# Optimization experiments

Hardware: AMD Instinct MI355X
Metric: run time of the kernel (lower is better)

Reference implementation:

```python
import jax, jax.numpy as jnp
import numpy as np

NUM_EXPERTS = 8
TOP_K = 2


def setup_inputs() -> dict:
    key = jax.random.key(0)
    k1, k2, k3, k4, k5 = jax.random.split(key, 5)
    B, S, H, F, E = 4, 2048, 1024, 4096, NUM_EXPERTS
    return {
        "hidden_states": jax.random.normal(k1, (B, S, H), dtype=jnp.float32),
        "gate_w": jax.random.normal(k2, (E, H), dtype=jnp.float32) * 0.02,
        "w1": jax.random.normal(k3, (E, F, H), dtype=jnp.float32) * 0.02,
        "w3": jax.random.normal(k4, (E, F, H), dtype=jnp.float32) * 0.02,
        "w2": jax.random.normal(k5, (E, H, F), dtype=jnp.float32) * 0.02,
    }


def reference(hidden_states, gate_w, w1, w3, w2):
    B, S, H = hidden_states.shape
    E = gate_w.shape[0]
    x = hidden_states.reshape(-1, H)  # [T, H]
    T = x.shape[0]

    # Router: logits -> fp32 softmax -> top-k -> renormalize (Mixtral)
    router_logits = x @ gate_w.T  # [T, E]
    probs = jax.nn.softmax(router_logits.astype(jnp.float32), axis=-1)
    top_w, top_idx = jax.lax.top_k(probs, TOP_K)  # [T, K]
    top_w = top_w / jnp.sum(top_w, axis=-1, keepdims=True)
    top_w = top_w.astype(x.dtype)

    # Combine weights per (token, expert); zero for unselected experts.
    comb = jnp.zeros((T, E), dtype=x.dtype).at[
        jnp.arange(T)[:, None], top_idx
    ].add(top_w)  # [T, E]

    out = jnp.zeros((T, H), dtype=x.dtype)
    for e in range(E):  # structural loop over distinct expert weights
        h = jax.nn.silu(x @ w1[e].T) * (x @ w3[e].T)  # [T, F]
        out = out + comb[:, e:e + 1] * (h @ w2[e].T)  # [T, H]

    return out.reshape(B, S, H), router_logits
```

## Files before the change

### kernel.cpp

```cpp
#include <hip/hip_runtime.h>
#include <hip/hip_bf16.h>
#include <stdint.h>

#define T_TOK 8192
#define H_DIM 1024
#define F_DIM 4096
#define NEXP  8
#define CAP        17408
#define CT128      136

typedef __attribute__((ext_vector_type(8))) short bf16x8;
typedef __attribute__((ext_vector_type(4))) float f32x4;

#define AS1 __attribute__((address_space(1)))
#define AS3 __attribute__((address_space(3)))

__device__ __forceinline__ void gload_lds16(const void* g, void* l) {
  __builtin_amdgcn_global_load_lds((const AS1 void*)g, (AS3 void*)l, 16, 0, 0);
}

struct TK { int i0, i1; float w0, w1; };

__global__ __launch_bounds__(256) void router_kernel(
    const float* __restrict__ x, const float* __restrict__ gw,
    float* __restrict__ logits, int* __restrict__ counts, TK* __restrict__ tk)
{
  const int lane = threadIdx.x & 63;
  const int t = blockIdx.x * 4 + (threadIdx.x >> 6);
  const float* xp = x + (size_t)t * H_DIM;
  float xr[16];
#pragma unroll
  for (int i = 0; i < 16; ++i) xr[i] = xp[lane + i * 64];
  float lg[NEXP];
#pragma unroll
  for (int e = 0; e < NEXP; ++e) {
    const float* gp = gw + e * H_DIM;
    float acc = 0.f;
#pragma unroll
    for (int i = 0; i < 16; ++i) acc += xr[i] * gp[lane + i * 64];
#pragma unroll
    for (int s = 32; s > 0; s >>= 1) acc += __shfl_xor(acc, s, 64);
    lg[e] = acc;
  }
  if (lane < NEXP) logits[(size_t)t * NEXP + lane] = lg[lane];
  if (lane == 0) {
    int i0 = 0; float m0 = lg[0];
#pragma unroll
    for (int e = 1; e < NEXP; ++e) if (lg[e] > m0) { m0 = lg[e]; i0 = e; }
    int i1 = -1; float m1 = -1e30f;
#pragma unroll
    for (int e = 0; e < NEXP; ++e) if (e != i0 && lg[e] > m1) { m1 = lg[e]; i1 = e; }
    float r = expf(m1 - m0);
    float w0 = 1.f / (1.f + r);
    float w1 = r / (1.f + r);
    TK v; v.i0 = i0; v.i1 = i1; v.w0 = w0; v.w1 = w1;
    tk[t] = v;
    atomicAdd(&counts[i0], 1);
    atomicAdd(&counts[i1], 1);
  }
}

__global__ __launch_bounds__(256) void scan_kernel(
    const int* __restrict__ counts, int* __restrict__ offs,
    int* __restrict__ cursor, int* __restrict__ tile_expert)
{
  __shared__ int so[NEXP + 1];
  const int tid = threadIdx.x;
  if (tid == 0) {
    int o = 0;
    for (int e = 0; e < NEXP; ++e) {
      so[e] = o; offs[e] = o; cursor[e] = o;
      o += (counts[e] + 127) & ~127;
    }
    so[NEXP] = o; offs[NEXP] = o;
  }
  __syncthreads();
  for (int ti = tid; ti < CT128; ti += 256) {
    int row = ti * 128;
    int e = NEXP - 1;
#pragma unroll
    for (int k = 0; k < NEXP; ++k)
      if (row >= so[k] && row < so[k + 1]) { e = k; break; }
    tile_expert[ti] = e;
  }
}

__global__ __launch_bounds__(256) void scatter_kernel(
    const TK* __restrict__ tk, int* __restrict__ cursor,
    int* __restrict__ pair_tok, float* __restrict__ pair_w,
    int2* __restrict__ inv)
{
  int t = blockIdx.x * 256 + threadIdx.x;
  if (t >= T_TOK) return;
  TK v = tk[t];
  int p0 = atomicAdd(&cursor[v.i0], 1);
  pair_tok[p0] = t; pair_w[p0] = v.w0;
  int p1 = atomicAdd(&cursor[v.i1], 1);
  pair_tok[p1] = t; pair_w[p1] = v.w1;
  inv[t] = make_int2(p0, p1);
}

union Pack8 { __hip_bfloat16 o[8]; uint4 u; };

__global__ __launch_bounds__(256) void gather_kernel(
    const float* __restrict__ x, const int* __restrict__ pair_tok,
    __hip_bfloat16* __restrict__ xg)
{
  int idx = blockIdx.x * 256 + threadIdx.x;
  int row = idx >> 7;
  int c8  = (idx & 127) << 3;
  int tok = pair_tok[row];
  const float4* src = reinterpret_cast<const float4*>(x + (size_t)tok * H_DIM + c8);
  float4 a = src[0], b = src[1];
  Pack8 pk;
  pk.o[0] = __float2bfloat16(a.x); pk.o[1] = __float2bfloat16(a.y);
  pk.o[2] = __float2bfloat16(a.z); pk.o[3] = __float2bfloat16(a.w);
  pk.o[4] = __float2bfloat16(b.x); pk.o[5] = __float2bfloat16(b.y);
  pk.o[6] = __float2bfloat16(b.z); pk.o[7] = __float2bfloat16(b.w);
  *reinterpret_cast<uint4*>(xg + (size_t)row * H_DIM + c8) = pk.u;
}

__global__ __launch_bounds__(256) void convert3_kernel(
    const float* __restrict__ w1, const float* __restrict__ w3,
    const float* __restrict__ w2, __hip_bfloat16* __restrict__ w1b,
    __hip_bfloat16* __restrict__ w3b, __hip_bfloat16* __restrict__ w2b)
{
  const long long nthr = 3ll * (1 << 22);
  for (long long idx = (long long)blockIdx.x * 256 + threadIdx.x; idx < nthr;
       idx += (long long)gridDim.x * 256) {
    int seg = (int)(idx >> 22);
    long long off = (idx & ((1 << 22) - 1)) * 8;
    const float* src = (seg == 0) ? w1 : (seg == 1) ? w3 : w2;
    __hip_bfloat16* dst = (seg == 0) ? w1b : (seg == 1) ? w3b : w2b;
    float4 a = *reinterpret_cast<const float4*>(src + off);
    float4 b = *reinterpret_cast<const float4*>(src + off + 4);
    Pack8 pk;
    pk.o[0] = __float2bfloat16(a.x); pk.o[1] = __float2bfloat16(a.y);
    pk.o[2] = __float2bfloat16(a.z); pk.o[3] = __float2bfloat16(a.w);
    pk.o[4] = __float2bfloat16(b.x); pk.o[5] = __float2bfloat16(b.y);
    pk.o[6] = __float2bfloat16(b.z); pk.o[7] = __float2bfloat16(b.w);
    *reinterpret_cast<uint4*>(dst + off) = pk.u;
  }
}


__global__ __launch_bounds__(256, 4) void gemm1_kernel(
    const __hip_bfloat16* __restrict__ xg,
    const __hip_bfloat16* __restrict__ w1b,
    const __hip_bfloat16* __restrict__ w3b,
    const int* __restrict__ tile_expert,
    __hip_bfloat16* __restrict__ h)
{
  __shared__ __hip_bfloat16 smem[16384];
  __hip_bfloat16* sA  = smem;
  __hip_bfloat16* sB1 = smem + 8192;
  __hip_bfloat16* sB3 = smem + 12288;

  const int n_  = blockIdx.x;
  const int tm  = n_ >> 6;
  const int tf  = n_ & 63;
  const int e   = tile_expert[tm];
  const int tid = threadIdx.x;

  const __hip_bfloat16* A  = xg  + (size_t)tm * 128 * H_DIM;
  const __hip_bfloat16* B1 = w1b + (size_t)e * F_DIM * H_DIM + (size_t)tf * 64 * H_DIM;
  const __hip_bfloat16* B3 = w3b + (size_t)e * F_DIM * H_DIM + (size_t)tf * 64 * H_DIM;

  const int rs  = tid >> 3;
  const int sl  = tid & 7;
  const int xsl = (sl ^ (rs & 7)) * 8;
  const int dst = rs * 64 + sl * 8;

  const int wv = tid >> 6, lane = tid & 63;
  const int wm = wv >> 1, wn = wv & 1;
  const int l16 = lane & 15, lk = lane >> 4;
  const int ps0 = ((0 + lk) ^ (l16 & 7)) * 8;
  const int ps1 = ((4 + lk) ^ (l16 & 7)) * 8;

  f32x4 acc1[4][2] = {};
  f32x4 acc3[4][2] = {};

  for (int kt = 0; kt < H_DIM / 64; ++kt) {
    __syncthreads();
    const int gk = kt * 64 + xsl;
#pragma unroll
    for (int c = 0; c < 4; ++c)
      gload_lds16(A + (size_t)(rs + 32 * c) * H_DIM + gk, &sA[c * 2048 + dst]);
#pragma unroll
    for (int c = 0; c < 2; ++c) {
      gload_lds16(B1 + (size_t)(rs + 32 * c) * H_DIM + gk, &sB1[c * 2048 + dst]);
      gload_lds16(B3 + (size_t)(rs + 32 * c) * H_DIM + gk, &sB3[c * 2048 + dst]);
    }
    __syncthreads();
#pragma unroll
    for (int ks = 0; ks < 2; ++ks) {
      const int ps = ks ? ps1 : ps0;
      bf16x8 a[4], b1[2], b3[2];
#pragma unroll
      for (int m = 0; m < 4; ++m)
        a[m] = *reinterpret_cast<const bf16x8*>(&sA[(wm * 64 + m * 16 + l16) * 64 + ps]);
#pragma unroll
      for (int nf = 0; nf < 2; ++nf) {
        b1[nf] = *reinterpret_cast<const bf16x8*>(&sB1[(wn * 32 + nf * 16 + l16) * 64 + ps]);
        b3[nf] = *reinterpret_cast<const bf16x8*>(&sB3[(wn * 32 + nf * 16 + l16) * 64 + ps]);
      }
#pragma unroll
      for (int m = 0; m < 4; ++m)
#pragma unroll
        for (int nf = 0; nf < 2; ++nf) {
          acc1[m][nf] = __builtin_amdgcn_mfma_f32_16x16x32_bf16(a[m], b1[nf], acc1[m][nf], 0, 0, 0);
          acc3[m][nf] = __builtin_amdgcn_mfma_f32_16x16x32_bf16(a[m], b3[nf], acc3[m][nf], 0, 0, 0);
        }
    }
  }

  __syncthreads();
#pragma unroll
  for (int m = 0; m < 4; ++m)
#pragma unroll
    for (int nf = 0; nf < 2; ++nf)
#pragma unroll
      for (int j = 0; j < 4; ++j) {
        int row = wm * 64 + m * 16 + lk * 4 + j;
        int col = wn * 32 + nf * 16 + l16;
        int phys = row * 64 + (((col >> 3) ^ (row & 7)) << 3) + (col & 7);
        float c1 = acc1[m][nf][j];
        float c3 = acc3[m][nf][j];
        float s  = c1 / (1.f + expf(-c1));
        smem[phys] = __float2bfloat16(s * c3);
      }
  __syncthreads();
  const uint4* s4 = reinterpret_cast<const uint4*>(smem);
  __hip_bfloat16* hp = h + (size_t)tm * 128 * F_DIM + (size_t)tf * 64;
#pragma unroll
  for (int i = 0; i < 4; ++i) {
    int c = i * 256 + tid;
    int row = c >> 3, sg = c & 7;
    *reinterpret_cast<uint4*>(hp + (size_t)row * F_DIM + sg * 8) =
        s4[row * 8 + (sg ^ (row & 7))];
  }
}

__global__ __launch_bounds__(256, 4) void gemm2_kernel(
    const __hip_bfloat16* __restrict__ h,
    const __hip_bfloat16* __restrict__ w2b,
    const int* __restrict__ tile_expert,
    const float* __restrict__ pair_w,
    __hip_bfloat16* __restrict__ y)
{
  __shared__ __hip_bfloat16 smem[16384];
  __hip_bfloat16* sA = smem;
  __hip_bfloat16* sB = smem + 8192;

  const int n_  = blockIdx.x;
  const int tn  = n_ & 7;
  const int tm  = n_ >> 3;
  const int e   = tile_expert[tm];
  const int tid = threadIdx.x;

  const __hip_bfloat16* A = h   + (size_t)tm * 128 * F_DIM;
  const __hip_bfloat16* B = w2b + (size_t)e * H_DIM * F_DIM + (size_t)tn * 128 * F_DIM;

  const int rs  = tid >> 3;
  const int sl  = tid & 7;
  const int xsl = (sl ^ (rs & 7)) * 8;
  const int dst = rs * 64 + sl * 8;

  const int wv = tid >> 6, lane = tid & 63;
  const int wm = wv >> 1, wn = wv & 1;
  const int l16 = lane & 15, lk = lane >> 4;
  const int ps0 = ((0 + lk) ^ (l16 & 7)) * 8;
  const int ps1 = ((4 + lk) ^ (l16 & 7)) * 8;

  f32x4 acc[4][4] = {};

  for (int kt = 0; kt < F_DIM / 64; ++kt) {
    __syncthreads();
    const int gk = kt * 64 + xsl;
#pragma unroll
    for (int c = 0; c < 4; ++c) {
      gload_lds16(A + (size_t)(rs + 32 * c) * F_DIM + gk, &sA[c * 2048 + dst]);
      gload_lds16(B + (size_t)(rs + 32 * c) * F_DIM + gk, &sB[c * 2048 + dst]);
    }
    __syncthreads();
#pragma unroll
    for (int ks = 0; ks < 2; ++ks) {
      const int ps = ks ? ps1 : ps0;
      bf16x8 a[4], b[4];
#pragma unroll
      for (int m = 0; m < 4; ++m)
        a[m] = *reinterpret_cast<const bf16x8*>(&sA[(wm * 64 + m * 16 + l16) * 64 + ps]);
#pragma unroll
      for (int nf = 0; nf < 4; ++nf)
        b[nf] = *reinterpret_cast<const bf16x8*>(&sB[(wn * 64 + nf * 16 + l16) * 64 + ps]);
#pragma unroll
      for (int m = 0; m < 4; ++m)
#pragma unroll
        for (int nf = 0; nf < 4; ++nf)
          acc[m][nf] = __builtin_amdgcn_mfma_f32_16x16x32_bf16(a[m], b[nf], acc[m][nf], 0, 0, 0);
    }
  }

  __syncthreads();
#pragma unroll
  for (int m = 0; m < 4; ++m)
#pragma unroll
    for (int j = 0; j < 4; ++j) {
      int row  = wm * 64 + m * 16 + lk * 4 + j;
      float w  = pair_w[tm * 128 + row];
#pragma unroll
      for (int nf = 0; nf < 4; ++nf) {
        int col  = wn * 64 + nf * 16 + l16;
        int phys = row * 128 + (((col >> 3) ^ (row & 7)) << 3) + (col & 7);
        smem[phys] = __float2bfloat16(w * acc[m][nf][j]);
      }
    }
  __syncthreads();
  const uint4* s4 = reinterpret_cast<const uint4*>(smem);
  __hip_bfloat16* yp = y + (size_t)tm * 128 * H_DIM + (size_t)tn * 128;
#pragma unroll
  for (int i = 0; i < 8; ++i) {
    int c = i * 256 + tid;
    int row = c >> 4, sg = c & 15;
    *reinterpret_cast<uint4*>(yp + (size_t)row * H_DIM + sg * 8) =
        s4[row * 16 + ((sg & 8) | ((sg ^ row) & 7))];
  }
}

__global__ __launch_bounds__(256) void combine_kernel(
    const __hip_bfloat16* __restrict__ y, const int2* __restrict__ inv,
    float* __restrict__ out)
{
  int idx = blockIdx.x * 256 + threadIdx.x;
  int t  = idx >> 7;
  int c8 = (idx & 127) << 3;
  int2 p = inv[t];
  union { uint4 u; __hip_bfloat16 o[8]; } a, b;
  a.u = *reinterpret_cast<const uint4*>(y + (size_t)p.x * H_DIM + c8);
  b.u = *reinterpret_cast<const uint4*>(y + (size_t)p.y * H_DIM + c8);
  float4 o0, o1;
  o0.x = __bfloat162float(a.o[0]) + __bfloat162float(b.o[0]);
  o0.y = __bfloat162float(a.o[1]) + __bfloat162float(b.o[1]);
  o0.z = __bfloat162float(a.o[2]) + __bfloat162float(b.o[2]);
  o0.w = __bfloat162float(a.o[3]) + __bfloat162float(b.o[3]);
  o1.x = __bfloat162float(a.o[4]) + __bfloat162float(b.o[4]);
  o1.y = __bfloat162float(a.o[5]) + __bfloat162float(b.o[5]);
  o1.z = __bfloat162float(a.o[6]) + __bfloat162float(b.o[6]);
  o1.w = __bfloat162float(a.o[7]) + __bfloat162float(b.o[7]);
  float* op = out + (size_t)t * H_DIM + c8;
  *reinterpret_cast<float4*>(op)     = o0;
  *reinterpret_cast<float4*>(op + 4) = o1;
}

#define WS_COUNTS   0
#define WS_CURSOR   32
#define WS_OFFS     64
#define WS_TILEEXP  128
#define WS_TK       1024
#define WS_PAIRTOK  132096
#define WS_PAIRW    201728
#define WS_ZERO_BYTES 271360
#define WS_INV      271360
#define WS_XG       336896ll
#define WS_W1       (WS_XG + 35651584ll)
#define WS_W3       (WS_W1 + 67108864ll)
#define WS_W2       (WS_W3 + 67108864ll)
#define WS_H        (WS_W2 + 67108864ll)
#define WS_Y        WS_XG

extern "C" void kernel_launch(void* const* d_in, const int* in_sizes, int n_in,
                              void* d_out, int out_size, void* d_ws, size_t ws_size,
                              hipStream_t stream) {
  const float* x  = (const float*)d_in[0];
  const float* gw = (const float*)d_in[1];
  const float* w1 = (const float*)d_in[2];
  const float* w3 = (const float*)d_in[3];
  const float* w2 = (const float*)d_in[4];
  float* out    = (float*)d_out;
  float* logits = out + (size_t)T_TOK * H_DIM;

  char* ws = (char*)d_ws;
  int*   counts   = (int*)(ws + WS_COUNTS);
  int*   cursor   = (int*)(ws + WS_CURSOR);
  int*   offs     = (int*)(ws + WS_OFFS);
  int*   tile_exp = (int*)(ws + WS_TILEEXP);
  TK*    tk       = (TK*)(ws + WS_TK);
  int*   pair_tok = (int*)(ws + WS_PAIRTOK);
  float* pair_w   = (float*)(ws + WS_PAIRW);
  int2*  inv      = (int2*)(ws + WS_INV);
  __hip_bfloat16* xg  = (__hip_bfloat16*)(ws + WS_XG);
  __hip_bfloat16* w1b = (__hip_bfloat16*)(ws + WS_W1);
  __hip_bfloat16* w3b = (__hip_bfloat16*)(ws + WS_W3);
  __hip_bfloat16* w2b = (__hip_bfloat16*)(ws + WS_W2);
  __hip_bfloat16* hbuf = (__hip_bfloat16*)(ws + WS_H);
  __hip_bfloat16* ybuf = (__hip_bfloat16*)(ws + WS_Y);

  hipMemsetAsync(d_ws, 0, WS_ZERO_BYTES, stream);

  convert3_kernel<<<8192, 256, 0, stream>>>(w1, w3, w2, w1b, w3b, w2b);

  router_kernel<<<T_TOK / 4, 256, 0, stream>>>(x, gw, logits, counts, tk);
  scan_kernel<<<1, 256, 0, stream>>>(counts, offs, cursor, tile_exp);
  scatter_kernel<<<T_TOK / 256, 256, 0, stream>>>(tk, cursor, pair_tok, pair_w, inv);
  gather_kernel<<<(CAP * 128) / 256, 256, 0, stream>>>(x, pair_tok, xg);

  gemm1_kernel<<<CT128 * (F_DIM / 64), 256, 0, stream>>>(
      xg, w1b, w3b, tile_exp, hbuf);
  gemm2_kernel<<<CT128 * (H_DIM / 128), 256, 0, stream>>>(
      hbuf, w2b, tile_exp, pair_w, ybuf);
  combine_kernel<<<(T_TOK * H_DIM / 8) / 256, 256, 0, stream>>>(ybuf, inv, out);
}
```

Before: 899.4 us.

## Split-K gemm2 into two halves and sum partials in combine kernel

Splits the second expert GEMM's K dimension (F=4096) into two halves, doubling the grid from 1088 to 2176 blocks. Each half writes its own bf16 partial output buffer, and the combine kernel now reads four partials per token instead of two. Block indices are also remapped so that consecutive blocks share groups of 8 M-tiles, which is meant to improve L2 reuse. The cost is double the y traffic, an extra bf16 rounding of each partial, and a second y buffer placed in the workspace after the first, which must fit in the existing allocation.

```diff
diff --git a/kernel.cpp b/kernel.cpp
--- a/kernel.cpp
+++ b/kernel.cpp
@@ -253,13 +253,18 @@
   __hip_bfloat16* sB = smem + 8192;
 
   const int n_  = blockIdx.x;
-  const int tn  = n_ & 7;
-  const int tm  = n_ >> 3;
+  const int r   = n_ & 7;
+  const int q   = n_ >> 3;
+  const int tm  = (q >> 4) * 8 + r;
+  const int s_  = q & 15;
+  const int tn  = s_ >> 1;
+  const int kh  = s_ & 1;
   const int e   = tile_expert[tm];
   const int tid = threadIdx.x;
 
-  const __hip_bfloat16* A = h   + (size_t)tm * 128 * F_DIM;
-  const __hip_bfloat16* B = w2b + (size_t)e * H_DIM * F_DIM + (size_t)tn * 128 * F_DIM;
+  const __hip_bfloat16* A = h   + (size_t)tm * 128 * F_DIM + (size_t)kh * 2048;
+  const __hip_bfloat16* B = w2b + (size_t)e * H_DIM * F_DIM + (size_t)tn * 128 * F_DIM
+                                + (size_t)kh * 2048;
 
   const int rs  = tid >> 3;
   const int sl  = tid & 7;
@@ -274,7 +279,7 @@
 
   f32x4 acc[4][4] = {};
 
-  for (int kt = 0; kt < F_DIM / 64; ++kt) {
+  for (int kt = 0; kt < 2048 / 64; ++kt) {
     __syncthreads();
     const int gk = kt * 64 + xsl;
 #pragma unroll
@@ -317,7 +322,8 @@
     }
   __syncthreads();
   const uint4* s4 = reinterpret_cast<const uint4*>(smem);
-  __hip_bfloat16* yp = y + (size_t)tm * 128 * H_DIM + (size_t)tn * 128;
+  __hip_bfloat16* yp = y + (size_t)kh * CAP * H_DIM
+                         + (size_t)tm * 128 * H_DIM + (size_t)tn * 128;
 #pragma unroll
   for (int i = 0; i < 8; ++i) {
     int c = i * 256 + tid;
@@ -335,21 +341,17 @@
   int t  = idx >> 7;
   int c8 = (idx & 127) << 3;
   int2 p = inv[t];
-  union { uint4 u; __hip_bfloat16 o[8]; } a, b;
-  a.u = *reinterpret_cast<const uint4*>(y + (size_t)p.x * H_DIM + c8);
-  b.u = *reinterpret_cast<const uint4*>(y + (size_t)p.y * H_DIM + c8);
-  float4 o0, o1;
-  o0.x = __bfloat162float(a.o[0]) + __bfloat162float(b.o[0]);
-  o0.y = __bfloat162float(a.o[1]) + __bfloat162float(b.o[1]);
-  o0.z = __bfloat162float(a.o[2]) + __bfloat162float(b.o[2]);
-  o0.w = __bfloat162float(a.o[3]) + __bfloat162float(b.o[3]);
-  o1.x = __bfloat162float(a.o[4]) + __bfloat162float(b.o[4]);
-  o1.y = __bfloat162float(a.o[5]) + __bfloat162float(b.o[5]);
-  o1.z = __bfloat162float(a.o[6]) + __bfloat162float(b.o[6]);
-  o1.w = __bfloat162float(a.o[7]) + __bfloat162float(b.o[7]);
+  const __hip_bfloat16* y1 = y + (size_t)CAP * H_DIM;
+  union { uint4 u; __hip_bfloat16 o[8]; } a, b, c, d;
+  a.u = *reinterpret_cast<const uint4*>(y  + (size_t)p.x * H_DIM + c8);
+  b.u = *reinterpret_cast<const uint4*>(y  + (size_t)p.y * H_DIM + c8);
+  c.u = *reinterpret_cast<const uint4*>(y1 + (size_t)p.x * H_DIM + c8);
+  d.u = *reinterpret_cast<const uint4*>(y1 + (size_t)p.y * H_DIM + c8);
   float* op = out + (size_t)t * H_DIM + c8;
-  *reinterpret_cast<float4*>(op)     = o0;
-  *reinterpret_cast<float4*>(op + 4) = o1;
+#pragma unroll
+  for (int i = 0; i < 8; ++i)
+    op[i] = __bfloat162float(a.o[i]) + __bfloat162float(b.o[i]) +
+            __bfloat162float(c.o[i]) + __bfloat162float(d.o[i]);
 }
 
 #define WS_COUNTS   0
@@ -406,7 +408,7 @@
 
   gemm1_kernel<<<CT128 * (F_DIM / 64), 256, 0, stream>>>(
       xg, w1b, w3b, tile_exp, hbuf);
-  gemm2_kernel<<<CT128 * (H_DIM / 128), 256, 0, stream>>>(
+  gemm2_kernel<<<CT128 * 16, 256, 0, stream>>>(
       hbuf, w2b, tile_exp, pair_w, ybuf);
   combine_kernel<<<(T_TOK * H_DIM / 8) / 256, 256, 0, stream>>>(ybuf, inv, out);
 }
```

After: 868.9 us. 1.04x faster.
